# Kernel optimization log

Measured on AMD Instinct MI355X. Metric: run time of the kernel, lower is better.

The kernel has to match this reference:

```python
import jax, jax.numpy as jnp
import numpy as np

N_INT4, N_INT8, K, GROUP = 6144, 2048, 8192, 128
N_TOTAL = N_INT4 + N_INT8
M = 16


def setup_inputs() -> dict:
    key = jax.random.key(0)
    ks = jax.random.split(key, 8)
    x = jax.random.normal(ks[0], (M, K), jnp.float32)
    # uint4 weights: values 0..15 (stored int32)
    w_int4 = jax.random.randint(ks[1], (N_INT4, K), 0, 16, jnp.int32)
    # group-wise scales [N_int4, K//group_size]
    s_int4 = jax.random.uniform(ks[2], (N_INT4, K // GROUP), jnp.float32, minval=0.005, maxval=0.02)
    # int8 weights stored in offset-128 form (w_int8 + 128 -> 0..255), as pack_for_marlin builds
    w_uint8 = jax.random.randint(ks[3], (N_INT8, K), 0, 256, jnp.int32)
    # per-channel int8 scales
    s_int8 = jax.random.uniform(ks[4], (N_INT8,), jnp.float32, minval=0.005, maxval=0.02)
    awq_scales = jax.random.uniform(ks[5], (K,), jnp.float32, minval=0.5, maxval=2.0)
    bias = jax.random.normal(ks[6], (N_TOTAL,), jnp.float32) * 0.01
    inv_perm = jax.random.permutation(ks[7], N_TOTAL).astype(jnp.int32)
    return dict(x=x, w_int4=w_int4, s_int4=s_int4, w_uint8=w_uint8, s_int8=s_int8,
                awq_scales=awq_scales, bias=bias, inv_perm=inv_perm, group_size=GROUP)


def reference(x, w_int4, s_int4, w_uint8, s_int8, awq_scales, bias, inv_perm, group_size):
    dt = x.dtype
    k = x.shape[-1]
    # AWQ input scaling (unfused path: x / awq_scales)
    x2 = x.reshape(-1, k) / awq_scales[None, :]
    sum_x = jnp.sum(x2, axis=1, keepdims=True)  # [M, 1]

    # Marlin uint4b8 dequant: (q - 8) * scale, group-wise scales for int4 rows
    s4_k = jnp.repeat(s_int4, group_size, axis=1)            # [N4, K]
    W4 = (w_int4.astype(dt) - 8.0) * s4_k                    # [N4, K]

    # int8 rows split into high/low nibbles with scales 16*s and s
    high = (w_uint8 >> 4) & 15
    low = w_uint8 & 15
    Wh = (high.astype(dt) - 8.0) * (16.0 * s_int8)[:, None]  # [N8, K]
    Wl = (low.astype(dt) - 8.0) * s_int8[:, None]            # [N8, K]

    Wc = jnp.concatenate([W4, Wh, Wl], axis=0)               # [N4+2*N8, K]
    y = x2 @ Wc.T                                            # marlin_gemm equivalent

    n4 = W4.shape[0]
    n8 = s_int8.shape[0]
    y4 = y[:, :n4]
    # int8 reconstruction: y_high + y_low + 8*s_int8*sum_x  == s_int8 * (x @ w_int8^T)
    y8 = y[:, n4:n4 + n8] + y[:, n4 + n8:] + (8.0 * s_int8)[None, :] * sum_x
    y_out = jnp.concatenate([y4, y8], axis=-1)[:, inv_perm] + bias[None, :]
    return y_out.reshape(*x.shape[:-1], n4 + n8)
```

## Files before the change

### kernel.cpp

```cpp
#include <hip/hip_runtime.h>
#include <hip/hip_bf16.h>

constexpr int K    = 8192;
constexpr int N4   = 6144;
constexpr int N8   = 2048;
constexpr int NT   = N4 + N8;
constexpr int NG   = K / 128;

typedef short  short8  __attribute__((ext_vector_type(8)));
typedef float  floatx4 __attribute__((ext_vector_type(4)));

__device__ inline short f2bf(float f) {
    __hip_bfloat16 h = __float2bfloat16(f);
    return __builtin_bit_cast(short, h);
}

__global__ void prep_kernel(const float* __restrict__ x,
                            const float* __restrict__ awq,
                            const int*   __restrict__ inv_perm,
                            short* __restrict__ x2bf,
                            int*   __restrict__ fwd) {
    const int tid  = blockIdx.x * blockDim.x + threadIdx.x;
    const int c    = tid >> 9;
    const int rem  = tid & 511;
    const int lane = rem >> 3;
    const int j    = rem & 7;
    const int m    = lane & 15;
    const int k    = c * 32 + (lane >> 4) * 8 + j;
    x2bf[tid] = f2bf(x[m * K + k] / awq[k]);
    if (tid < NT) fwd[inv_perm[tid]] = tid;
}

__global__ __launch_bounds__(256)
void qgemv_kernel(const short* __restrict__ xf,
                  const int*   __restrict__ w4,
                  const float* __restrict__ s4,
                  const int*   __restrict__ w8,
                  const float* __restrict__ s8,
                  const int*   __restrict__ fwd,
                  const float* __restrict__ bias,
                  float* __restrict__ out) {
    __shared__ float lds[4 * 256];

    const int t    = threadIdx.x;
    const int lane = t & 63;
    const int w    = t >> 6;
    const int nb   = blockIdx.x * 16;
    const int i    = lane & 15;
    const int q    = lane >> 4;
    const int row  = nb + i;

    const bool is4 = (nb < N4);
    const int*   wp = (is4 ? (w4 + (size_t)row * K)
                           : (w8 + (size_t)(row - N4) * K))
                      + (size_t)w * 2048 + q * 8;
    const short* xw = xf + (size_t)w * 64 * 512 + lane * 8;
    const float* sp = is4 ? (s4 + (size_t)row * NG + w * 16) : nullptr;

    floatx4 acc = {0.f, 0.f, 0.f, 0.f};

    int4   wbA[8], wbB[8];
    short8 abA[4], abB[4];
    float  sA = 0.f, sB = 0.f;

    auto loadg = [&](int g, int4* wb, short8* ab, float& s) {
        #pragma unroll
        for (int c = 0; c < 4; ++c) {
            const size_t co = (size_t)(g * 4 + c);
            wb[2 * c]     = *(const int4*)(wp + co * 32);
            wb[2 * c + 1] = *(const int4*)(wp + co * 32 + 4);
            ab[c]         = *(const short8*)(xw + co * 512);
        }
        if (is4) s = sp[g];
    };

    auto compg = [&](const int4* wb, const short8* ab, float s) {
        const float sc = is4 ? s : 1.f;
        const float sb = is4 ? -8.f * s : -128.f;
        #pragma unroll
        for (int c = 0; c < 4; ++c) {
            const int4 wa = wb[2 * c];
            const int4 wz = wb[2 * c + 1];
            short8 bf;
            bf[0] = f2bf((float)wa.x * sc + sb);
            bf[1] = f2bf((float)wa.y * sc + sb);
            bf[2] = f2bf((float)wa.z * sc + sb);
            bf[3] = f2bf((float)wa.w * sc + sb);
            bf[4] = f2bf((float)wz.x * sc + sb);
            bf[5] = f2bf((float)wz.y * sc + sb);
            bf[6] = f2bf((float)wz.z * sc + sb);
            bf[7] = f2bf((float)wz.w * sc + sb);
            acc = __builtin_amdgcn_mfma_f32_16x16x32_bf16(ab[c], bf, acc, 0, 0, 0);
        }
    };

    loadg(0, wbA, abA, sA);
    #pragma unroll 1
    for (int g = 0; g < 16; g += 2) {
        const int g1 = (g + 1 < 16) ? g + 1 : 15;
        loadg(g1, wbB, abB, sB);
        compg(wbA, abA, sA);
        const int g2 = (g + 2 < 16) ? g + 2 : 15;
        loadg(g2, wbA, abA, sA);
        compg(wbB, abB, sB);
    }

    #pragma unroll
    for (int r = 0; r < 4; ++r)
        lds[w * 256 + (q * 4 + r) * 16 + i] = acc[r];
    __syncthreads();

    {
        const int m  = t >> 4;
        const int i2 = t & 15;
        const float v = lds[0 * 256 + t] + lds[1 * 256 + t]
                      + lds[2 * 256 + t] + lds[3 * 256 + t];
        const int n  = nb + i2;
        const float sc = is4 ? 1.f : s8[n - N4];
        const int d  = fwd[n];
        out[(size_t)m * NT + d] = v * sc + bias[d];
    }
}

extern "C" void kernel_launch(void* const* d_in, const int* in_sizes, int n_in,
                              void* d_out, int out_size, void* d_ws, size_t ws_size,
                              hipStream_t stream) {
    const float* x        = (const float*)d_in[0];
    const int*   w_int4   = (const int*)  d_in[1];
    const float* s_int4   = (const float*)d_in[2];
    const int*   w_uint8  = (const int*)  d_in[3];
    const float* s_int8   = (const float*)d_in[4];
    const float* awq      = (const float*)d_in[5];
    const float* bias     = (const float*)d_in[6];
    const int*   inv_perm = (const int*)  d_in[7];

    short* x2bf = (short*)d_ws;
    int*   fwd  = (int*)((char*)d_ws + (size_t)16 * K * sizeof(short));

    prep_kernel<<<(16 * K) / 256, 256, 0, stream>>>(x, awq, inv_perm, x2bf, fwd);
    qgemv_kernel<<<NT / 16, 256, 0, stream>>>(x2bf, w_int4, s_int4,
                                              w_uint8, s_int8, fwd, bias,
                                              (float*)d_out);
}
```

Before: 337.3 us.

## Split K across eight waves and apply group scale after MFMA

Blocks grow from 256 to 512 threads, so each of the eight waves covers 1024 K elements and the LDS reduction sums eight partials. Dequantization now only adds a constant offset before the bf16 conversion. The per-group scale, or the per-row int8 scale, is applied to a fresh MFMA partial accumulator per group of two chunks. This removes a multiply per weight element and exposes more memory parallelism per block, at the cost of extra accumulate ops and a slightly different rounding order.

New measurement: 368.1 us. 9.1% more time.

```diff
diff --git a/kernel.cpp b/kernel.cpp
--- a/kernel.cpp
+++ b/kernel.cpp
@@ -31,7 +31,21 @@
     if (tid < NT) fwd[inv_perm[tid]] = tid;
 }
 
-__global__ __launch_bounds__(256)
+__device__ inline floatx4 chunk_mfma(int4 wa, int4 wb, short8 xv, float off,
+                                     floatx4 cin) {
+    short8 bf;
+    bf[0] = f2bf((float)wa.x + off);
+    bf[1] = f2bf((float)wa.y + off);
+    bf[2] = f2bf((float)wa.z + off);
+    bf[3] = f2bf((float)wa.w + off);
+    bf[4] = f2bf((float)wb.x + off);
+    bf[5] = f2bf((float)wb.y + off);
+    bf[6] = f2bf((float)wb.z + off);
+    bf[7] = f2bf((float)wb.w + off);
+    return __builtin_amdgcn_mfma_f32_16x16x32_bf16(xv, bf, cin, 0, 0, 0);
+}
+
+__global__ __launch_bounds__(512)
 void qgemv_kernel(const short* __restrict__ xf,
                   const int*   __restrict__ w4,
                   const float* __restrict__ s4,
@@ -40,7 +54,7 @@
                   const int*   __restrict__ fwd,
                   const float* __restrict__ bias,
                   float* __restrict__ out) {
-    __shared__ float lds[4 * 256];
+    __shared__ float lds[8 * 256];
 
     const int t    = threadIdx.x;
     const int lane = t & 63;
@@ -50,75 +64,72 @@
     const int q    = lane >> 4;
     const int row  = nb + i;
 
-    const bool is4 = (nb < N4);
+    const bool  is4 = (nb < N4);
+    const float off = is4 ? -8.f : -128.f;
+
     const int*   wp = (is4 ? (w4 + (size_t)row * K)
                            : (w8 + (size_t)(row - N4) * K))
-                      + (size_t)w * 2048 + q * 8;
-    const short* xw = xf + (size_t)w * 64 * 512 + lane * 8;
-    const float* sp = is4 ? (s4 + (size_t)row * NG + w * 16) : nullptr;
+                      + w * 1024 + q * 8;
+    const short* xw = xf + ((size_t)w * 32) * 512 + lane * 8;
+    const float* sp = s4 + (size_t)row * NG + w * 8;
+    const float  s8row = is4 ? 0.f : s8[row - N4];
 
     floatx4 acc = {0.f, 0.f, 0.f, 0.f};
 
-    int4   wbA[8], wbB[8];
-    short8 abA[4], abB[4];
-    float  sA = 0.f, sB = 0.f;
+    int4   wA0, wA1, wA2, wA3, wB0, wB1, wB2, wB3;
+    short8 xA0, xA1, xB0, xB1;
+    float  sA, sB;
 
-    auto loadg = [&](int g, int4* wb, short8* ab, float& s) {
-        #pragma unroll
-        for (int c = 0; c < 4; ++c) {
-            const size_t co = (size_t)(g * 4 + c);
-            wb[2 * c]     = *(const int4*)(wp + co * 32);
-            wb[2 * c + 1] = *(const int4*)(wp + co * 32 + 4);
-            ab[c]         = *(const short8*)(xw + co * 512);
-        }
-        if (is4) s = sp[g];
-    };
+#define LOADSTAGE(S, W0, W1, W2, W3, X0, X1, SS)                     \
+    do {                                                             \
+        const int c_ = 2 * (S);                                      \
+        W0 = *(const int4*)(wp + (size_t)c_ * 32);                   \
+        W1 = *(const int4*)(wp + (size_t)c_ * 32 + 4);               \
+        W2 = *(const int4*)(wp + (size_t)c_ * 32 + 32);              \
+        W3 = *(const int4*)(wp + (size_t)c_ * 32 + 36);              \
+        X0 = *(const short8*)(xw + (size_t)c_ * 512);                \
+        X1 = *(const short8*)(xw + (size_t)c_ * 512 + 512);          \
+        SS = is4 ? sp[(S) >> 1] : s8row;                             \
+    } while (0)
 
-    auto compg = [&](const int4* wb, const short8* ab, float s) {
-        const float sc = is4 ? s : 1.f;
-        const float sb = is4 ? -8.f * s : -128.f;
-        #pragma unroll
-        for (int c = 0; c < 4; ++c) {
-            const int4 wa = wb[2 * c];
-            const int4 wz = wb[2 * c + 1];
-            short8 bf;
-            bf[0] = f2bf((float)wa.x * sc + sb);
-            bf[1] = f2bf((float)wa.y * sc + sb);
-            bf[2] = f2bf((float)wa.z * sc + sb);
-            bf[3] = f2bf((float)wa.w * sc + sb);
-            bf[4] = f2bf((float)wz.x * sc + sb);
-            bf[5] = f2bf((float)wz.y * sc + sb);
-            bf[6] = f2bf((float)wz.z * sc + sb);
-            bf[7] = f2bf((float)wz.w * sc + sb);
-            acc = __builtin_amdgcn_mfma_f32_16x16x32_bf16(ab[c], bf, acc, 0, 0, 0);
-        }
-    };
+#define COMPSTAGE(W0, W1, W2, W3, X0, X1, SS)                        \
+    do {                                                             \
+        floatx4 g_ = chunk_mfma(W0, W1, X0, off,                     \
+                                (floatx4){0.f, 0.f, 0.f, 0.f});      \
+        g_ = chunk_mfma(W2, W3, X1, off, g_);                        \
+        acc[0] += (SS) * g_[0];                                      \
+        acc[1] += (SS) * g_[1];                                      \
+        acc[2] += (SS) * g_[2];                                      \
+        acc[3] += (SS) * g_[3];                                      \
+    } while (0)
 
-    loadg(0, wbA, abA, sA);
+    LOADSTAGE(0, wA0, wA1, wA2, wA3, xA0, xA1, sA);
     #pragma unroll 1
-    for (int g = 0; g < 16; g += 2) {
-        const int g1 = (g + 1 < 16) ? g + 1 : 15;
-        loadg(g1, wbB, abB, sB);
-        compg(wbA, abA, sA);
-        const int g2 = (g + 2 < 16) ? g + 2 : 15;
-        loadg(g2, wbA, abA, sA);
-        compg(wbB, abB, sB);
+    for (int s = 0; s < 16; s += 2) {
+        const int s1 = (s + 1 < 16) ? s + 1 : 15;
+        LOADSTAGE(s1, wB0, wB1, wB2, wB3, xB0, xB1, sB);
+        COMPSTAGE(wA0, wA1, wA2, wA3, xA0, xA1, sA);
+        const int s2 = (s + 2 < 16) ? s + 2 : 15;
+        LOADSTAGE(s2, wA0, wA1, wA2, wA3, xA0, xA1, sA);
+        COMPSTAGE(wB0, wB1, wB2, wB3, xB0, xB1, sB);
     }
+#undef LOADSTAGE
+#undef COMPSTAGE
 
     #pragma unroll
     for (int r = 0; r < 4; ++r)
         lds[w * 256 + (q * 4 + r) * 16 + i] = acc[r];
     __syncthreads();
 
-    {
+    if (t < 256) {
+        float v = 0.f;
+        #pragma unroll
+        for (int ww = 0; ww < 8; ++ww) v += lds[ww * 256 + t];
         const int m  = t >> 4;
         const int i2 = t & 15;
-        const float v = lds[0 * 256 + t] + lds[1 * 256 + t]
-                      + lds[2 * 256 + t] + lds[3 * 256 + t];
         const int n  = nb + i2;
-        const float sc = is4 ? 1.f : s8[n - N4];
         const int d  = fwd[n];
-        out[(size_t)m * NT + d] = v * sc + bias[d];
+        out[(size_t)m * NT + d] = v + bias[d];
     }
 }
 
@@ -138,7 +149,7 @@
     int*   fwd  = (int*)((char*)d_ws + (size_t)16 * K * sizeof(short));
 
     prep_kernel<<<(16 * K) / 256, 256, 0, stream>>>(x, awq, inv_perm, x2bf, fwd);
-    qgemv_kernel<<<NT / 16, 256, 0, stream>>>(x2bf, w_int4, s_int4,
+    qgemv_kernel<<<NT / 16, 512, 0, stream>>>(x2bf, w_int4, s_int4,
                                               w_uint8, s_int8, fwd, bias,
                                               (float*)d_out);
 }
```
